# Kernel tuning notes

Hardware: AMD Instinct MI355X
Metric: run time of the kernel (lower is better)

Reference implementation:

```python
import jax, jax.numpy as jnp
import numpy as np

B, S, HID, NH = 2, 2048, 2048, 16
ROPE, NOPE, VDIM = 64, 64, 128
QHEAD = ROPE + NOPE            # 128
QLORA = HID // 3               # 682
KVLORA = HID // 8              # 256
THETA = 128000.0
SCALE = 1.0 / np.sqrt(QHEAD)   # deepseek softmax_scale = q_head_dim**-0.5
EPS = 1e-6


def rmsnorm(x, w):
    var = jnp.mean(x.astype(jnp.float32) ** 2, axis=-1, keepdims=True)
    return (x.astype(jnp.float32) * jax.lax.rsqrt(var + EPS)).astype(x.dtype) * w


def rope_cos_sin(seq, dim, theta):
    inv = 1.0 / (theta ** (jnp.arange(0, dim, 2, dtype=jnp.float32) / dim))
    t = jnp.arange(seq, dtype=jnp.float32)
    freqs = jnp.outer(t, inv)                      # [S, dim/2]
    emb = jnp.concatenate([freqs, freqs], axis=-1)  # [S, dim]
    return jnp.cos(emb), jnp.sin(emb)


def apply_rope(x, cos, sin):
    # deepseek interleave: view(b,h,s,d/2,2).transpose(-1,-2).reshape, then rotate_half rope
    b, h, s, d = x.shape
    x = x.reshape(b, h, s, d // 2, 2).transpose(0, 1, 2, 4, 3).reshape(b, h, s, d)
    x1, x2 = jnp.split(x, 2, axis=-1)
    rot = jnp.concatenate([-x2, x1], axis=-1)
    return x * cos + rot * sin


def setup_inputs() -> dict:
    key = jax.random.key(0)
    ks = jax.random.split(key, 8)
    s = lambda fan_in: 1.0 / np.sqrt(fan_in)
    return {
        "x":        jax.random.normal(ks[0], (B, S, HID), jnp.float32),
        "q_a_w":    jax.random.normal(ks[1], (HID, QLORA), jnp.float32) * s(HID),
        "q_a_ln_w": jnp.ones((QLORA,), jnp.float32),
        "q_b_w":    jax.random.normal(ks[2], (QLORA, NH * QHEAD), jnp.float32) * s(QLORA),
        "kv_a_w":   jax.random.normal(ks[3], (HID, KVLORA + ROPE), jnp.float32) * s(HID),
        "kv_a_ln_w": jnp.ones((KVLORA,), jnp.float32),
        "kv_b_w":   jax.random.normal(ks[4], (KVLORA, NH * (NOPE + VDIM)), jnp.float32) * s(KVLORA),
        "o_w":      jax.random.normal(ks[5], (NH * VDIM, HID), jnp.float32) * s(NH * VDIM),
    }


def reference(x, q_a_w, q_a_ln_w, q_b_w, kv_a_w, kv_a_ln_w, kv_b_w, o_w):
    b, s, _ = x.shape
    # Q: low-rank down-proj -> RMSNorm -> up-proj
    q = rmsnorm(x @ q_a_w, q_a_ln_w) @ q_b_w               # [b,s,NH*QHEAD]
    q = q.reshape(b, s, NH, QHEAD).transpose(0, 2, 1, 3)   # [b,NH,s,QHEAD]
    q_nope, q_pe = q[..., :NOPE], q[..., NOPE:]
    # KV: compressed latent + shared rope key
    ckv_kpe = x @ kv_a_w                                   # [b,s,KVLORA+ROPE]
    ckv, k_pe = ckv_kpe[..., :KVLORA], ckv_kpe[..., KVLORA:]
    k_pe = k_pe.reshape(b, 1, s, ROPE)                     # shared across heads
    kv = rmsnorm(ckv, kv_a_ln_w) @ kv_b_w                  # [b,s,NH*(NOPE+VDIM)]
    kv = kv.reshape(b, s, NH, NOPE + VDIM).transpose(0, 2, 1, 3)
    k_nope, v = kv[..., :NOPE], kv[..., NOPE:]             # [b,NH,s,NOPE], [b,NH,s,VDIM]
    # decoupled RoPE on the rope split only
    cos, sin = rope_cos_sin(s, ROPE, THETA)
    q_pe = apply_rope(q_pe, cos, sin)
    k_pe = apply_rope(k_pe, cos, sin)
    qf = jnp.concatenate([q_nope, q_pe], axis=-1)          # [b,NH,s,QHEAD]
    kf = jnp.concatenate([k_nope, jnp.broadcast_to(k_pe, (b, NH, s, ROPE))], axis=-1)
    scores = jnp.einsum('bhqd,bhkd->bhqk', qf, kf) * SCALE
    causal = jnp.tril(jnp.ones((s, s), bool))
    scores = jnp.where(causal, scores, jnp.float32(-1e9))
    attn = jax.nn.softmax(scores.astype(jnp.float32), axis=-1).astype(qf.dtype)
    out = jnp.einsum('bhqk,bhkd->bhqd', attn, v)           # [b,NH,s,VDIM]
    out = out.transpose(0, 2, 1, 3).reshape(b, s, NH * VDIM)
    return out @ o_w                                       # [b,s,HID]
```

## Files before the change

kernel.cpp:

```cpp
#include <hip/hip_runtime.h>
#include <hip/hip_bf16.h>

typedef __attribute__((ext_vector_type(8))) short short8;
typedef __attribute__((ext_vector_type(4))) float f32x4;

using bf16 = __hip_bfloat16;

static constexpr int B_ = 2, S_ = 2048, HID_ = 2048, NH_ = 16;
static constexpr int ROPE_ = 64, VDIM_ = 128, QHEAD_ = 128;
static constexpr int QLORA_ = 682, KVLORA_ = 256;
static constexpr int QLORA_P = 704;
static constexpr int NQA_P = 768;
static constexpr int NKVA_P = 384;
static constexpr int NA_ = NQA_P + NKVA_P;
static constexpr float THETA_ = 128000.0f;
static constexpr float SCALE_ = 0.08838834764831845f;
static constexpr float SCL2_ = 0.08838834764831845f * 1.4426950408889634f;
static constexpr float EPS_ = 1e-6f;
static constexpr int BS_ = B_ * S_;

__device__ __forceinline__ void gl2lds16(const void* g, void* l) {
    __builtin_amdgcn_global_load_lds(
        (const __attribute__((address_space(1))) unsigned int*)g,
        (__attribute__((address_space(3))) unsigned int*)l, 16, 0, 0);
}

struct bf16x4_s { bf16 x, y, z, w; };

__device__ __forceinline__ float bfLo(unsigned int u) { return __uint_as_float(u << 16); }
__device__ __forceinline__ float bfHi(unsigned int u) { return __uint_as_float(u & 0xffff0000u); }

struct TD { const float* src; bf16* dst; const float* colw;
            int Ksrc, Nsrc, Kpad, tilesX, off, perm; };
struct TDs { TD d[5]; };
static constexpr int PREP_TILES = 8576;

__global__ void k_prep(TDs P, const float* __restrict__ x, bf16* __restrict__ xb,
                       float* __restrict__ ct, float* __restrict__ st,
                       float* __restrict__ sums) {
    __shared__ float tile[32][33];
    if (blockIdx.x >= PREP_TILES) {
        int bid = blockIdx.x - PREP_TILES;
        int t = threadIdx.y * 32 + threadIdx.x;
        if (bid < 8192) {
            int i = bid * 256 + t;
            float4 v = reinterpret_cast<const float4*>(x)[i];
            bf16x4_s o;
            o.x = __float2bfloat16(v.x); o.y = __float2bfloat16(v.y);
            o.z = __float2bfloat16(v.z); o.w = __float2bfloat16(v.w);
            reinterpret_cast<bf16x4_s*>(xb)[i] = o;
        } else if (bid < 8192 + 256) {
            int idx = (bid - 8192) * 256 + t;
            int tpos = idx >> 5, j = idx & 31;
            float inv = expf(-(float)j * (logf(THETA_) / 32.0f));
            float f = (float)tpos * inv;
            ct[idx] = cosf(f);
            st[idx] = sinf(f);
        } else {
            int z = bid - (8192 + 256);
            reinterpret_cast<float4*>(sums)[z * 256 + t] = make_float4(0.f, 0.f, 0.f, 0.f);
        }
        return;
    }
    int flat = blockIdx.x;
    int di = 0;
    #pragma unroll
    for (int i = 1; i < 5; ++i) if (flat >= P.d[i].off) di = i;
    TD d = P.d[di];
    int local = flat - d.off;
    int xt = local % d.tilesX, yt = local / d.tilesX;
    int kb = xt * 32, nb = yt * 32;
    int tx = threadIdx.x, ty = threadIdx.y;
    #pragma unroll
    for (int i = 0; i < 32; i += 8) {
        int k = kb + ty + i, n = nb + tx;
        float v = (k < d.Ksrc && n < d.Nsrc) ? d.src[(size_t)k * d.Nsrc + n] : 0.0f;
        if (d.colw && k < d.Ksrc) v *= d.colw[k];
        tile[ty + i][tx] = v;
    }
    __syncthreads();
    int u = ty * 32 + tx;
    int kp = u & 15;
    int nl = u >> 4;
    #pragma unroll
    for (int half = 0; half < 2; ++half) {
        int n_loc = nl + 16 * half;
        int n = nb + n_loc;
        int nd = n;
        if (d.perm) {
            int h = n / 192, dd = n - h * 192;
            nd = (dd < 64) ? h * 64 + dd : 1024 + h * 128 + (dd - 64);
        }
        bf16 lo = __float2bfloat16(tile[2 * kp][n_loc]);
        bf16 hi = __float2bfloat16(tile[2 * kp + 1][n_loc]);
        unsigned int pk = (unsigned int)*reinterpret_cast<unsigned short*>(&lo) |
                          ((unsigned int)*reinterpret_cast<unsigned short*>(&hi) << 16);
        *reinterpret_cast<unsigned int*>(d.dst + (size_t)nd * d.Kpad + kb + 2 * kp) = pk;
    }
}

#define GEMM_VARS                                                                        \
    __shared__ bf16 As[128 * 64];                                                        \
    __shared__ bf16 Bs[128 * 64];                                                        \
    const int t = threadIdx.x;                                                           \
    const int lane = t & 63, w = t >> 6;                                                 \
    const int l15 = lane & 15, l4 = lane >> 4;                                           \
    const int wr = (w >> 1) * 64, wc = (w & 1) * 64;

#define GEMM_CORE(Aptr, Bptr, LDA, LDB, KDIM, M0V, N0V)                                  \
    const int m0 = (M0V), n0 = (N0V);                                                    \
    f32x4 acc[4][4] = {};                                                                \
    for (int k0 = 0; k0 < (KDIM); k0 += 64) {                                            \
        _Pragma("unroll")                                                                \
        for (int i = 0; i < 4; ++i) {                                                    \
            int cid = t + i * 256;                                                       \
            int row = cid >> 3;                                                          \
            int ch = (cid & 7) ^ (row & 7);                                              \
            gl2lds16((Aptr) + (size_t)(m0 + row) * (LDA) + k0 + ch * 8,                  \
                     reinterpret_cast<char*>(As) + cid * 16);                            \
            gl2lds16((Bptr) + (size_t)(n0 + row) * (LDB) + k0 + ch * 8,                  \
                     reinterpret_cast<char*>(Bs) + cid * 16);                            \
        }                                                                                \
        __syncthreads();                                                                 \
        _Pragma("unroll")                                                                \
        for (int kk = 0; kk < 2; ++kk) {                                                 \
            short8 a[4], b[4];                                                           \
            _Pragma("unroll")                                                            \
            for (int m = 0; m < 4; ++m) {                                                \
                int row = wr + m * 16 + l15;                                             \
                int ch = (kk * 4 + l4) ^ (row & 7);                                      \
                a[m] = *reinterpret_cast<const short8*>(                                 \
                    reinterpret_cast<const char*>(As) + row * 128 + ch * 16);            \
            }                                                                            \
            _Pragma("unroll")                                                            \
            for (int n = 0; n < 4; ++n) {                                                \
                int row = wc + n * 16 + l15;                                             \
                int ch = (kk * 4 + l4) ^ (row & 7);                                      \
                b[n] = *reinterpret_cast<const short8*>(                                 \
                    reinterpret_cast<const char*>(Bs) + row * 128 + ch * 16);            \
            }                                                                            \
            _Pragma("unroll")                                                            \
            for (int m = 0; m < 4; ++m)                                                  \
                _Pragma("unroll")                                                        \
                for (int n = 0; n < 4; ++n)                                              \
                    acc[m][n] = __builtin_amdgcn_mfma_f32_16x16x32_bf16(a[m], b[n],      \
                                                                       acc[m][n], 0, 0, 0); \
        }                                                                                \
        __syncthreads();                                                                 \
    }

template <typename OutT>
__launch_bounds__(256)
__global__ void gemm_bt(const bf16* __restrict__ A, const bf16* __restrict__ Bt,
                        OutT* __restrict__ C, int K, int lda, int ldb, int ldc)
{
    GEMM_VARS
    GEMM_CORE(A, Bt, lda, ldb, K, blockIdx.y * 128, blockIdx.x * 128)
    #pragma unroll
    for (int m = 0; m < 4; ++m)
        #pragma unroll
        for (int n = 0; n < 4; ++n)
            #pragma unroll
            for (int j = 0; j < 4; ++j) {
                int r = m0 + wr + m * 16 + l4 * 4 + j;
                int c = n0 + wc + n * 16 + l15;
                float v = acc[m][n][j];
                if constexpr (sizeof(OutT) == 2) C[(size_t)r * ldc + c] = __float2bfloat16(v);
                else                             C[(size_t)r * ldc + c] = v;
            }
}

__launch_bounds__(256)
__global__ void gemm_a(const bf16* __restrict__ A, const bf16* __restrict__ Bt,
                       bf16* __restrict__ qac,
                       const float* __restrict__ ct, const float* __restrict__ st,
                       float* __restrict__ qsum, float* __restrict__ ksum,
                       bf16* __restrict__ kr)
{
    GEMM_VARS
    GEMM_CORE(A, Bt, HID_, HID_, HID_, blockIdx.y * 128, blockIdx.x * 128)
    if (n0 < 1024) {
        #pragma unroll
        for (int m = 0; m < 4; ++m)
            #pragma unroll
            for (int n = 0; n < 4; ++n)
                #pragma unroll
                for (int j = 0; j < 4; ++j) {
                    int r = m0 + wr + m * 16 + l4 * 4 + j;
                    int c = n0 + wc + n * 16 + l15;
                    qac[(size_t)r * NA_ + c] = __float2bfloat16(acc[m][n][j]);
                }
        float* dst = (n0 < 768) ? qsum : ksum;
        #pragma unroll
        for (int m = 0; m < 4; ++m)
            #pragma unroll
            for (int j = 0; j < 4; ++j) {
                float v = acc[m][0][j] * acc[m][0][j] + acc[m][1][j] * acc[m][1][j]
                        + acc[m][2][j] * acc[m][2][j] + acc[m][3][j] * acc[m][3][j];
                v += __shfl_xor(v, 1); v += __shfl_xor(v, 2);
                v += __shfl_xor(v, 4); v += __shfl_xor(v, 8);
                if (l15 == 0) atomicAdd(&dst[m0 + wr + m * 16 + l4 * 4 + j], v);
            }
    } else if (wc == 0) {
        #pragma unroll
        for (int m = 0; m < 4; ++m)
            #pragma unroll
            for (int n = 0; n < 4; ++n)
                #pragma unroll
                for (int j = 0; j < 4; ++j) {
                    int r = m0 + wr + m * 16 + l4 * 4 + j;
                    int p = n * 16 + l15;
                    int jj = p >> 1, odd = p & 1;
                    float v = acc[m][n][j];
                    float pr = __shfl_xor(v, 1);
                    float e0 = odd ? pr : v, e1 = odd ? v : pr;
                    int s = r & (S_ - 1);
                    float c_ = ct[s * 32 + jj], s_ = st[s * 32 + jj];
                    float ov = odd ? (e1 * c_ + e0 * s_) : (e0 * c_ - e1 * s_);
                    kr[(size_t)r * 64 + (odd ? 32 : 0) + jj] = __float2bfloat16(ov);
                }
    }
}

__launch_bounds__(256)
__global__ void gemm_up(const bf16* __restrict__ qac, const bf16* __restrict__ qb_wt,
                        const float* __restrict__ ct, const float* __restrict__ st,
                        const float* __restrict__ qsum, bf16* __restrict__ Qf,
                        const bf16* __restrict__ kvb_wt, const float* __restrict__ ksum,
                        bf16* __restrict__ knope, bf16* __restrict__ Vt)
{
    GEMM_VARS
    if (blockIdx.x < 16) {
        GEMM_CORE(qac, qb_wt, NA_, QLORA_P, QLORA_P, blockIdx.y * 128, blockIdx.x * 128)
        (void)n0;
        const int h = blockIdx.x;
        if (wc == 0) {
            #pragma unroll
            for (int m = 0; m < 4; ++m) {
                int rb = m0 + wr + m * 16 + l4 * 4;
                float q4[4];
                #pragma unroll
                for (int j = 0; j < 4; ++j)
                    q4[j] = rsqrtf(qsum[rb + j] * (1.0f / (float)QLORA_) + EPS_) * SCL2_;
                #pragma unroll
                for (int n = 0; n < 4; ++n)
                    #pragma unroll
                    for (int j = 0; j < 4; ++j) {
                        int r = rb + j;
                        int c = n * 16 + l15;
                        int s = r & (S_ - 1), bq = r >> 11;
                        Qf[((size_t)(bq * NH_ + h) * S_ + s) * 128 + c] =
                            __float2bfloat16(acc[m][n][j] * q4[j]);
                    }
            }
        } else {
            #pragma unroll
            for (int m = 0; m < 4; ++m) {
                int rb = m0 + wr + m * 16 + l4 * 4;
                float q4[4];
                #pragma unroll
                for (int j = 0; j < 4; ++j)
                    q4[j] = rsqrtf(qsum[rb + j] * (1.0f / (float)QLORA_) + EPS_) * SCL2_;
                #pragma unroll
                for (int n = 0; n < 4; ++n)
                    #pragma unroll
                    for (int j = 0; j < 4; ++j) {
                        int r = rb + j;
                        int p = n * 16 + l15;
                        int jj = p >> 1, odd = p & 1;
                        float v = acc[m][n][j];
                        float pr = __shfl_xor(v, 1);
                        float e0 = odd ? pr : v, e1 = odd ? v : pr;
                        int s = r & (S_ - 1), bq = r >> 11;
                        float c_ = ct[s * 32 + jj], s_ = st[s * 32 + jj];
                        float ov = odd ? (e1 * c_ + e0 * s_) : (e0 * c_ - e1 * s_);
                        int c_out = 64 + (odd ? 32 : 0) + jj;
                        Qf[((size_t)(bq * NH_ + h) * S_ + s) * 128 + c_out] =
                            __float2bfloat16(ov * q4[j]);
                    }
            }
        }
    } else {
        GEMM_CORE(qac + NQA_P, kvb_wt, NA_, KVLORA_, KVLORA_, blockIdx.y * 128,
                  (blockIdx.x - 16) * 128)
        if (n0 < 1024) {
            #pragma unroll
            for (int m = 0; m < 4; ++m) {
                int rb = m0 + wr + m * 16 + l4 * 4;
                float k4[4];
                #pragma unroll
                for (int j = 0; j < 4; ++j)
                    k4[j] = rsqrtf(ksum[rb + j] * (1.0f / (float)KVLORA_) + EPS_);
                #pragma unroll
                for (int n = 0; n < 4; ++n)
                    #pragma unroll
                    for (int j = 0; j < 4; ++j) {
                        int c = n0 + wc + n * 16 + l15;
                        knope[(size_t)(rb + j) * 1024 + c] =
                            __float2bfloat16(acc[m][n][j] * k4[j]);
                    }
            }
        } else {
            const int h = (n0 - 1024) >> 7;
            const int bq = m0 >> 11;
            const int bh = bq * NH_ + h;
            #pragma unroll
            for (int m = 0; m < 4; ++m) {
                int rb = m0 + wr + m * 16 + l4 * 4;
                int s = rb & (S_ - 1);
                float k4[4];
                #pragma unroll
                for (int j = 0; j < 4; ++j)
                    k4[j] = rsqrtf(ksum[rb + j] * (1.0f / (float)KVLORA_) + EPS_);
                #pragma unroll
                for (int n = 0; n < 4; ++n) {
                    int cl = wc + n * 16 + l15;
                    ushort4 pk;
                    {
                        bf16 h0 = __float2bfloat16(acc[m][n][0] * k4[0]);
                        bf16 h1 = __float2bfloat16(acc[m][n][1] * k4[1]);
                        bf16 h2 = __float2bfloat16(acc[m][n][2] * k4[2]);
                        bf16 h3 = __float2bfloat16(acc[m][n][3] * k4[3]);
                        pk.x = *reinterpret_cast<unsigned short*>(&h0);
                        pk.y = *reinterpret_cast<unsigned short*>(&h1);
                        pk.z = *reinterpret_cast<unsigned short*>(&h2);
                        pk.w = *reinterpret_cast<unsigned short*>(&h3);
                    }
                    *reinterpret_cast<ushort4*>(Vt + ((size_t)bh * 128 + cl) * S_ + s) = pk;
                }
            }
        }
    }
}

__launch_bounds__(512, 4)
__global__ void k_flash(const bf16* __restrict__ Qf, const bf16* __restrict__ knope,
                        const bf16* __restrict__ kr, const bf16* __restrict__ Vt,
                        bf16* __restrict__ attn_out)
{
    __shared__ bf16 Ks[64 * 128];
    __shared__ bf16 Vs[128 * 64];
    __shared__ bf16 Ps[8][16 * 64];

    const int t = threadIdx.x, lane = t & 63, w = t >> 6;
    const int l15 = lane & 15, l4 = lane >> 4;
    const int pi = blockIdx.y;
    const int bh = blockIdx.x;
    const int b = bh >> 4, h = bh & 15;
    const int strip = (w < 4) ? (31 - pi) : pi;
    const int r0 = strip * 64 + (w & 3) * 16;
    const int NT = 32 - pi;

    short8 qa_[4];
    {
        const bf16* qrow = Qf + ((size_t)bh * S_ + r0 + l15) * 128;
        #pragma unroll
        for (int kk = 0; kk < 4; ++kk)
            qa_[kk] = *reinterpret_cast<const short8*>(qrow + kk * 32 + l4 * 8);
    }

    const bf16 *kSrc0, *kSrc1, *vSrc0, *vSrc1;
    size_t kStp0, kStp1;
    {
        int cid = t, row = cid >> 4, ch = (cid & 15) ^ (row & 7);
        kSrc0 = (ch < 8) ? knope + (size_t)(b * S_ + row) * 1024 + h * 64 + ch * 8
                         : kr + (size_t)(b * S_ + row) * 64 + (ch - 8) * 8;
        kStp0 = (ch < 8) ? (size_t)64 * 1024 : (size_t)64 * 64;
    }
    {
        int cid = t + 512, row = cid >> 4, ch = (cid & 15) ^ (row & 7);
        kSrc1 = (ch < 8) ? knope + (size_t)(b * S_ + row) * 1024 + h * 64 + ch * 8
                         : kr + (size_t)(b * S_ + row) * 64 + (ch - 8) * 8;
        kStp1 = (ch < 8) ? (size_t)64 * 1024 : (size_t)64 * 64;
    }
    {
        const bf16* Vg = Vt + (size_t)bh * 128 * S_;
        int cid = t, row = cid >> 3, ch = (cid & 7) ^ (row & 7);
        vSrc0 = Vg + (size_t)row * S_ + ch * 8;
        cid = t + 512; row = cid >> 3; ch = (cid & 7) ^ (row & 7);
        vSrc1 = Vg + (size_t)row * S_ + ch * 8;
    }
    auto stage = [&]() {
        gl2lds16(kSrc0, reinterpret_cast<char*>(Ks) + t * 16);
        gl2lds16(kSrc1, reinterpret_cast<char*>(Ks) + (t + 512) * 16);
        gl2lds16(vSrc0, reinterpret_cast<char*>(Vs) + t * 16);
        gl2lds16(vSrc1, reinterpret_cast<char*>(Vs) + (t + 512) * 16);
        kSrc0 += kStp0; kSrc1 += kStp1; vSrc0 += 64; vSrc1 += 64;
    };

    stage();

    f32x4 o[8] = {};
    float m_r = -1e30f, l_r = 0.f;

    for (int kb = 0; kb < NT; ++kb) {
        const int k0 = kb * 64;
        __syncthreads();

        if (k0 <= r0 + 15) {
            f32x4 sfr[4] = {};
            __builtin_amdgcn_s_setprio(1);
            #pragma unroll
            for (int kk = 0; kk < 4; ++kk) {
                short8 kf[4];
                #pragma unroll
                for (int m = 0; m < 4; ++m) {
                    int row = m * 16 + l15;
                    int ch = (kk * 4 + l4) ^ (row & 7);
                    kf[m] = *reinterpret_cast<const short8*>(
                        reinterpret_cast<const char*>(Ks) + row * 256 + ch * 16);
                }
                #pragma unroll
                for (int m = 0; m < 4; ++m)
                    sfr[m] = __builtin_amdgcn_mfma_f32_16x16x32_bf16(kf[m], qa_[kk], sfr[m], 0, 0, 0);
            }
            __builtin_amdgcn_s_setprio(0);

            const int qrow = r0 + l15;
            if (k0 + 63 > r0) {
                #pragma unroll
                for (int m = 0; m < 4; ++m) {
                    int kbase = k0 + m * 16 + l4 * 4;
                    #pragma unroll
                    for (int j = 0; j < 4; ++j)
                        if (kbase + j > qrow) sfr[m][j] = -1e30f;
                }
            }

            float rm;
            {
                float a0 = fmaxf(fmaxf(sfr[0][0], sfr[0][1]), fmaxf(sfr[0][2], sfr[0][3]));
                float a1 = fmaxf(fmaxf(sfr[1][0], sfr[1][1]), fmaxf(sfr[1][2], sfr[1][3]));
                float a2 = fmaxf(fmaxf(sfr[2][0], sfr[2][1]), fmaxf(sfr[2][2], sfr[2][3]));
                float a3 = fmaxf(fmaxf(sfr[3][0], sfr[3][1]), fmaxf(sfr[3][2], sfr[3][3]));
                rm = fmaxf(fmaxf(a0, a1), fmaxf(a2, a3));
            }
            rm = fmaxf(rm, __shfl_xor(rm, 16));
            rm = fmaxf(rm, __shfl_xor(rm, 32));

            if (__ballot(rm > m_r + 8.0f)) {
                float mn = fmaxf(m_r, rm);
                float alpha = exp2f(m_r - mn);
                m_r = mn;
                l_r *= alpha;
                float aj[4];
                #pragma unroll
                for (int j = 0; j < 4; ++j) aj[j] = __shfl(alpha, l4 * 4 + j);
                #pragma unroll
                for (int n = 0; n < 8; ++n)
                    #pragma unroll
                    for (int j = 0; j < 4; ++j) o[n][j] *= aj[j];
            }

            char* pb = reinterpret_cast<char*>(Ps[w]);
            float rs = 0.f;
            #pragma unroll
            for (int m = 0; m < 4; ++m) {
                float p0 = exp2f(sfr[m][0] - m_r);
                float p1 = exp2f(sfr[m][1] - m_r);
                float p2 = exp2f(sfr[m][2] - m_r);
                float p3 = exp2f(sfr[m][3] - m_r);
                rs += (p0 + p1) + (p2 + p3);
                union { __hip_bfloat162 h; unsigned int u; } cl, ch2;
                cl.h  = __float22bfloat162_rn(make_float2(p0, p1));
                ch2.h = __float22bfloat162_rn(make_float2(p2, p3));
                int kloc = m * 16 + l4 * 4;
                int chnk = (kloc >> 3) ^ (l15 & 7);
                uint2 pk2; pk2.x = cl.u; pk2.y = ch2.u;
                *reinterpret_cast<uint2*>(pb + l15 * 128 + chnk * 16 + (kloc & 7) * 2) = pk2;
            }
            rs += __shfl_xor(rs, 16);
            rs += __shfl_xor(rs, 32);
            l_r += rs;

            __builtin_amdgcn_s_setprio(1);
            #pragma unroll
            for (int kk = 0; kk < 2; ++kk) {
                int pch = (kk * 4 + l4) ^ (l15 & 7);
                short8 pa = *reinterpret_cast<const short8*>(pb + l15 * 128 + pch * 16);
                #pragma unroll
                for (int n = 0; n < 8; ++n) {
                    int row = n * 16 + l15;
                    int ch = (kk * 4 + l4) ^ (row & 7);
                    short8 vb = *reinterpret_cast<const short8*>(
                        reinterpret_cast<const char*>(Vs) + row * 128 + ch * 16);
                    o[n] = __builtin_amdgcn_mfma_f32_16x16x32_bf16(pa, vb, o[n], 0, 0, 0);
                }
            }
            __builtin_amdgcn_s_setprio(0);
        }
        __syncthreads();
        if (kb + 1 < NT) stage();
    }

    float rj[4];
    #pragma unroll
    for (int j = 0; j < 4; ++j) rj[j] = __builtin_amdgcn_rcpf(__shfl(l_r, l4 * 4 + j));
    size_t obase = ((size_t)(b * S_) + r0) * (size_t)(NH_ * VDIM_) + h * VDIM_;
    #pragma unroll
    for (int n = 0; n < 8; ++n)
        #pragma unroll
        for (int j = 0; j < 4; ++j) {
            int r = l4 * 4 + j;
            int c = n * 16 + l15;
            attn_out[obase + (size_t)r * (NH_ * VDIM_) + c] = __float2bfloat16(o[n][j] * rj[j]);
        }
}

extern "C" void kernel_launch(void* const* d_in, const int* in_sizes, int n_in,
                              void* d_out, int out_size, void* d_ws, size_t ws_size,
                              hipStream_t stream)
{
    (void)in_sizes; (void)n_in; (void)out_size;
    const float* x       = (const float*)d_in[0];
    const float* q_a_w   = (const float*)d_in[1];
    const float* q_a_ln  = (const float*)d_in[2];
    const float* q_b_w   = (const float*)d_in[3];
    const float* kv_a_w  = (const float*)d_in[4];
    const float* kv_a_ln = (const float*)d_in[5];
    const float* kv_b_w  = (const float*)d_in[6];
    const float* o_w     = (const float*)d_in[7];
    float* out = (float*)d_out;

    char* ws = (char*)d_ws;
    size_t off = 0;
    auto alloc = [&](size_t bytes) -> char* {
        char* p = ws + off;
        off += (bytes + 255) & ~(size_t)255;
        return p;
    };

    bf16* xb     = (bf16*)alloc((size_t)BS_ * HID_ * 2);
    bf16* a_wt   = (bf16*)alloc((size_t)NA_ * HID_ * 2);
    bf16* qb_wt  = (bf16*)alloc((size_t)2048 * QLORA_P * 2);
    bf16* kvb_wt = (bf16*)alloc((size_t)3072 * KVLORA_ * 2);
    bf16* ow_t   = (bf16*)alloc((size_t)2048 * 2048 * 2);
    float* ct    = (float*)alloc((size_t)S_ * 32 * 4);
    float* st    = (float*)alloc((size_t)S_ * 32 * 4);
    bf16* qac    = (bf16*)alloc((size_t)BS_ * NA_ * 2);
    float* qsum  = (float*)alloc((size_t)8192 * 4);
    float* ksum  = qsum + BS_;
    bf16* kr     = (bf16*)alloc((size_t)BS_ * 64 * 2);
    bf16* knope  = (bf16*)alloc((size_t)BS_ * 1024 * 2);
    bf16* Vt     = (bf16*)alloc((size_t)BS_ * 2048 * 2);
    bf16* attn   = (bf16*)alloc((size_t)BS_ * 2048 * 2);

    bf16* Qf = xb;

    if (ws_size < off) return;

    TDs P;
    P.d[0] = TD{ q_a_w,  a_wt,                     nullptr, 2048,  682, 2048, 64,    0, 0 };
    P.d[1] = TD{ kv_a_w, a_wt + (size_t)NQA_P*2048,nullptr, 2048,  320, 2048, 64, 1536, 0 };
    P.d[2] = TD{ q_b_w,  qb_wt,                    q_a_ln,   682, 2048,  704, 22, 2304, 0 };
    P.d[3] = TD{ kv_b_w, kvb_wt,                   kv_a_ln,  256, 3072,  256,  8, 3712, 1 };
    P.d[4] = TD{ o_w,    ow_t,                     nullptr, 2048, 2048, 2048, 64, 4480, 0 };
    k_prep<<<PREP_TILES + 8192 + 256 + 8, dim3(32, 8), 0, stream>>>(P, x, xb, ct, st, qsum);

    gemm_a<<<dim3(NA_ / 128, BS_ / 128), 256, 0, stream>>>(xb, a_wt, qac, ct, st,
                                                           qsum, ksum, kr);

    gemm_up<<<dim3(16 + 24, BS_ / 128), 256, 0, stream>>>(qac, qb_wt, ct, st, qsum, Qf,
                                                          kvb_wt, ksum, knope, Vt);

    k_flash<<<dim3(B_ * NH_, 16), 512, 0, stream>>>(Qf, knope, kr, Vt, attn);

    gemm_bt<float><<<dim3(2048 / 128, BS_ / 128), 256, 0, stream>>>(attn, ow_t, out,
                                                                    HID_, HID_, HID_, 2048);
}
```

Measured before the change: 216.7 us.

## Software-pipeline flash attention with double-buffered K/V and overlapped QK and softmax

Double-buffers the K and V tiles in shared memory and restructures the key loop so the QK^T MFMAs for tile t run in the same step as the softmax and PV MFMAs for tile t-1. Staging of the next K tile and the current V tile is issued ahead of use. The goal is to hide load latency and interleave matrix and scalar work within a wave. In exchange, LDS use per block roughly doubles for K and V, and a second score fragment raises register pressure, both of which can cut occupancy or cause spills.

```diff
diff --git a/kernel.cpp b/kernel.cpp
--- a/kernel.cpp
+++ b/kernel.cpp
@@ -338,8 +338,8 @@
                         const bf16* __restrict__ kr, const bf16* __restrict__ Vt,
                         bf16* __restrict__ attn_out)
 {
-    __shared__ bf16 Ks[64 * 128];
-    __shared__ bf16 Vs[128 * 64];
+    __shared__ bf16 Ks[2][64 * 128];
+    __shared__ bf16 Vs[2][128 * 64];
     __shared__ bf16 Ps[8][16 * 64];
 
     const int t = threadIdx.x, lane = t & 63, w = t >> 6;
@@ -380,118 +380,134 @@
         cid = t + 512; row = cid >> 3; ch = (cid & 7) ^ (row & 7);
         vSrc1 = Vg + (size_t)row * S_ + ch * 8;
     }
-    auto stage = [&]() {
-        gl2lds16(kSrc0, reinterpret_cast<char*>(Ks) + t * 16);
-        gl2lds16(kSrc1, reinterpret_cast<char*>(Ks) + (t + 512) * 16);
-        gl2lds16(vSrc0, reinterpret_cast<char*>(Vs) + t * 16);
-        gl2lds16(vSrc1, reinterpret_cast<char*>(Vs) + (t + 512) * 16);
-        kSrc0 += kStp0; kSrc1 += kStp1; vSrc0 += 64; vSrc1 += 64;
+    auto stageK = [&](int buf) {
+        gl2lds16(kSrc0, reinterpret_cast<char*>(Ks[buf]) + t * 16);
+        gl2lds16(kSrc1, reinterpret_cast<char*>(Ks[buf]) + (t + 512) * 16);
+        kSrc0 += kStp0; kSrc1 += kStp1;
     };
-
-    stage();
+    auto stageV = [&](int buf) {
+        gl2lds16(vSrc0, reinterpret_cast<char*>(Vs[buf]) + t * 16);
+        gl2lds16(vSrc1, reinterpret_cast<char*>(Vs[buf]) + (t + 512) * 16);
+        vSrc0 += 64; vSrc1 += 64;
+    };
 
     f32x4 o[8] = {};
     float m_r = -1e30f, l_r = 0.f;
-
-    for (int kb = 0; kb < NT; ++kb) {
-        const int k0 = kb * 64;
+    f32x4 sA[4], sB[4];
+
+    auto S1 = [&](int tt, f32x4 (&sfr)[4]) {
+        if (tt * 64 > r0 + 15) return;
+        #pragma unroll
+        for (int m = 0; m < 4; ++m) sfr[m] = f32x4{0.f, 0.f, 0.f, 0.f};
+        const char* kb_ = reinterpret_cast<const char*>(Ks[tt & 1]);
+        __builtin_amdgcn_s_setprio(1);
+        #pragma unroll
+        for (int kk = 0; kk < 4; ++kk) {
+            short8 kf[4];
+            #pragma unroll
+            for (int m = 0; m < 4; ++m) {
+                int row = m * 16 + l15;
+                int ch = (kk * 4 + l4) ^ (row & 7);
+                kf[m] = *reinterpret_cast<const short8*>(kb_ + row * 256 + ch * 16);
+            }
+            #pragma unroll
+            for (int m = 0; m < 4; ++m)
+                sfr[m] = __builtin_amdgcn_mfma_f32_16x16x32_bf16(kf[m], qa_[kk], sfr[m], 0, 0, 0);
+        }
+        __builtin_amdgcn_s_setprio(0);
+    };
+
+    auto FIN = [&](int tt, f32x4 (&sfr)[4]) {
+        const int k0 = tt * 64;
+        if (k0 > r0 + 15) return;
+        const int qrow = r0 + l15;
+        if (k0 + 63 > r0) {
+            #pragma unroll
+            for (int m = 0; m < 4; ++m) {
+                int kbase = k0 + m * 16 + l4 * 4;
+                #pragma unroll
+                for (int j = 0; j < 4; ++j)
+                    if (kbase + j > qrow) sfr[m][j] = -1e30f;
+            }
+        }
+        float rm;
+        {
+            float a0 = fmaxf(fmaxf(sfr[0][0], sfr[0][1]), fmaxf(sfr[0][2], sfr[0][3]));
+            float a1 = fmaxf(fmaxf(sfr[1][0], sfr[1][1]), fmaxf(sfr[1][2], sfr[1][3]));
+            float a2 = fmaxf(fmaxf(sfr[2][0], sfr[2][1]), fmaxf(sfr[2][2], sfr[2][3]));
+            float a3 = fmaxf(fmaxf(sfr[3][0], sfr[3][1]), fmaxf(sfr[3][2], sfr[3][3]));
+            rm = fmaxf(fmaxf(a0, a1), fmaxf(a2, a3));
+        }
+        rm = fmaxf(rm, __shfl_xor(rm, 16));
+        rm = fmaxf(rm, __shfl_xor(rm, 32));
+        if (__ballot(rm > m_r + 8.0f)) {
+            float mn = fmaxf(m_r, rm);
+            float alpha = exp2f(m_r - mn);
+            m_r = mn;
+            l_r *= alpha;
+            float aj[4];
+            #pragma unroll
+            for (int j = 0; j < 4; ++j) aj[j] = __shfl(alpha, l4 * 4 + j);
+            #pragma unroll
+            for (int n = 0; n < 8; ++n)
+                #pragma unroll
+                for (int j = 0; j < 4; ++j) o[n][j] *= aj[j];
+        }
+        char* pb = reinterpret_cast<char*>(Ps[w]);
+        float rs = 0.f;
+        #pragma unroll
+        for (int m = 0; m < 4; ++m) {
+            float p0 = exp2f(sfr[m][0] - m_r);
+            float p1 = exp2f(sfr[m][1] - m_r);
+            float p2 = exp2f(sfr[m][2] - m_r);
+            float p3 = exp2f(sfr[m][3] - m_r);
+            rs += (p0 + p1) + (p2 + p3);
+            union { __hip_bfloat162 h; unsigned int u; } cl, ch2;
+            cl.h  = __float22bfloat162_rn(make_float2(p0, p1));
+            ch2.h = __float22bfloat162_rn(make_float2(p2, p3));
+            int kloc = m * 16 + l4 * 4;
+            int chnk = (kloc >> 3) ^ (l15 & 7);
+            uint2 pk2; pk2.x = cl.u; pk2.y = ch2.u;
+            *reinterpret_cast<uint2*>(pb + l15 * 128 + chnk * 16 + (kloc & 7) * 2) = pk2;
+        }
+        rs += __shfl_xor(rs, 16);
+        rs += __shfl_xor(rs, 32);
+        l_r += rs;
+        const char* vb_ = reinterpret_cast<const char*>(Vs[tt & 1]);
+        __builtin_amdgcn_s_setprio(1);
+        #pragma unroll
+        for (int kk = 0; kk < 2; ++kk) {
+            int pch = (kk * 4 + l4) ^ (l15 & 7);
+            short8 pa = *reinterpret_cast<const short8*>(pb + l15 * 128 + pch * 16);
+            #pragma unroll
+            for (int n = 0; n < 8; ++n) {
+                int row = n * 16 + l15;
+                int ch = (kk * 4 + l4) ^ (row & 7);
+                short8 vb = *reinterpret_cast<const short8*>(vb_ + row * 128 + ch * 16);
+                o[n] = __builtin_amdgcn_mfma_f32_16x16x32_bf16(pa, vb, o[n], 0, 0, 0);
+            }
+        }
+        __builtin_amdgcn_s_setprio(0);
+    };
+
+    auto ITER = [&](int tt, f32x4 (&cur)[4], f32x4 (&prv)[4]) {
+        if (tt + 1 < NT) stageK((tt + 1) & 1);
+        stageV(tt & 1);
+        S1(tt, cur);
+        if (tt > 0) FIN(tt - 1, prv);
         __syncthreads();
-
-        if (k0 <= r0 + 15) {
-            f32x4 sfr[4] = {};
-            __builtin_amdgcn_s_setprio(1);
-            #pragma unroll
-            for (int kk = 0; kk < 4; ++kk) {
-                short8 kf[4];
-                #pragma unroll
-                for (int m = 0; m < 4; ++m) {
-                    int row = m * 16 + l15;
-                    int ch = (kk * 4 + l4) ^ (row & 7);
-                    kf[m] = *reinterpret_cast<const short8*>(
-                        reinterpret_cast<const char*>(Ks) + row * 256 + ch * 16);
-                }
-                #pragma unroll
-                for (int m = 0; m < 4; ++m)
-                    sfr[m] = __builtin_amdgcn_mfma_f32_16x16x32_bf16(kf[m], qa_[kk], sfr[m], 0, 0, 0);
-            }
-            __builtin_amdgcn_s_setprio(0);
-
-            const int qrow = r0 + l15;
-            if (k0 + 63 > r0) {
-                #pragma unroll
-                for (int m = 0; m < 4; ++m) {
-                    int kbase = k0 + m * 16 + l4 * 4;
-                    #pragma unroll
-                    for (int j = 0; j < 4; ++j)
-                        if (kbase + j > qrow) sfr[m][j] = -1e30f;
-                }
-            }
-
-            float rm;
-            {
-                float a0 = fmaxf(fmaxf(sfr[0][0], sfr[0][1]), fmaxf(sfr[0][2], sfr[0][3]));
-                float a1 = fmaxf(fmaxf(sfr[1][0], sfr[1][1]), fmaxf(sfr[1][2], sfr[1][3]));
-                float a2 = fmaxf(fmaxf(sfr[2][0], sfr[2][1]), fmaxf(sfr[2][2], sfr[2][3]));
-                float a3 = fmaxf(fmaxf(sfr[3][0], sfr[3][1]), fmaxf(sfr[3][2], sfr[3][3]));
-                rm = fmaxf(fmaxf(a0, a1), fmaxf(a2, a3));
-            }
-            rm = fmaxf(rm, __shfl_xor(rm, 16));
-            rm = fmaxf(rm, __shfl_xor(rm, 32));
-
-            if (__ballot(rm > m_r + 8.0f)) {
-                float mn = fmaxf(m_r, rm);
-                float alpha = exp2f(m_r - mn);
-                m_r = mn;
-                l_r *= alpha;
-                float aj[4];
-                #pragma unroll
-                for (int j = 0; j < 4; ++j) aj[j] = __shfl(alpha, l4 * 4 + j);
-                #pragma unroll
-                for (int n = 0; n < 8; ++n)
-                    #pragma unroll
-                    for (int j = 0; j < 4; ++j) o[n][j] *= aj[j];
-            }
-
-            char* pb = reinterpret_cast<char*>(Ps[w]);
-            float rs = 0.f;
-            #pragma unroll
-            for (int m = 0; m < 4; ++m) {
-                float p0 = exp2f(sfr[m][0] - m_r);
-                float p1 = exp2f(sfr[m][1] - m_r);
-                float p2 = exp2f(sfr[m][2] - m_r);
-                float p3 = exp2f(sfr[m][3] - m_r);
-                rs += (p0 + p1) + (p2 + p3);
-                union { __hip_bfloat162 h; unsigned int u; } cl, ch2;
-                cl.h  = __float22bfloat162_rn(make_float2(p0, p1));
-                ch2.h = __float22bfloat162_rn(make_float2(p2, p3));
-                int kloc = m * 16 + l4 * 4;
-                int chnk = (kloc >> 3) ^ (l15 & 7);
-                uint2 pk2; pk2.x = cl.u; pk2.y = ch2.u;
-                *reinterpret_cast<uint2*>(pb + l15 * 128 + chnk * 16 + (kloc & 7) * 2) = pk2;
-            }
-            rs += __shfl_xor(rs, 16);
-            rs += __shfl_xor(rs, 32);
-            l_r += rs;
-
-            __builtin_amdgcn_s_setprio(1);
-            #pragma unroll
-            for (int kk = 0; kk < 2; ++kk) {
-                int pch = (kk * 4 + l4) ^ (l15 & 7);
-                short8 pa = *reinterpret_cast<const short8*>(pb + l15 * 128 + pch * 16);
-                #pragma unroll
-                for (int n = 0; n < 8; ++n) {
-                    int row = n * 16 + l15;
-                    int ch = (kk * 4 + l4) ^ (row & 7);
-                    short8 vb = *reinterpret_cast<const short8*>(
-                        reinterpret_cast<const char*>(Vs) + row * 128 + ch * 16);
-                    o[n] = __builtin_amdgcn_mfma_f32_16x16x32_bf16(pa, vb, o[n], 0, 0, 0);
-                }
-            }
-            __builtin_amdgcn_s_setprio(0);
-        }
-        __syncthreads();
-        if (kb + 1 < NT) stage();
-    }
+    };
+
+    stageK(0);
+    __syncthreads();
+
+    int tc = 0;
+    for (; tc + 1 < NT; tc += 2) {
+        ITER(tc,     sA, sB);
+        ITER(tc + 1, sB, sA);
+    }
+    if (tc < NT) { ITER(tc, sA, sB); FIN(tc, sA); }
+    else         { FIN(NT - 1, sB); }
 
     float rj[4];
     #pragma unroll
```

Result: slower. 240.3 us (+10.9%).
